# Kernel tuning notes

Measured on AMD Instinct MI355X. Metric: run time of the kernel, lower is better.

Reference implementation:

```python
import jax, jax.numpy as jnp
import numpy as np

ALPHA = 1.0

def setup_inputs() -> dict:
    key = jax.random.key(0)
    kx, kd = jax.random.split(key)
    B, L, D = 64, 256, 512
    x = jax.random.normal(kx, (B, L, D), dtype=jnp.float32)
    duration = jax.random.randint(kd, (B, L), 0, 8, dtype=jnp.int32)
    max_length = 1792  # L * max_duration
    return {"x": x, "duration": duration, "max_length": max_length}

def reference(x, duration, max_length):
    B, L, D = x.shape
    # round(duration * alpha) -> integer durations
    d = jnp.round(duration.astype(jnp.float32) * ALPHA).astype(jnp.int32)
    # rows with all-zero durations get one frame (original picks a random
    # position; we deterministically use position 0)
    row_sum = d.sum(axis=1)  # [B]
    d = jnp.where((row_sum == 0)[:, None] & (jnp.arange(L) == 0)[None, :], 1, d)
    # cumulative end offsets per phoneme: cum[b, j] = sum_{k<=j} d[b, k]
    cum = jnp.cumsum(d, axis=1)  # [B, L]
    t = jnp.arange(max_length)   # [T]
    # output frame t belongs to phoneme j where cum[j-1] <= t < cum[j]
    idx = jax.vmap(lambda c: jnp.searchsorted(c, t, side='right'))(cum)  # [B, T]
    idx = jnp.clip(idx, 0, L - 1)
    out = jnp.take_along_axis(x, idx[:, :, None], axis=1)  # [B, T, D]
    # zero-pad beyond each sequence's total length
    mask = (t[None, :] < cum[:, -1:]).astype(x.dtype)  # [B, T]
    out = out * mask[:, :, None]
    return out, max_length
```

## Files before the change

kernel.cpp:

```cpp
#include <hip/hip_runtime.h>


#define BB 64
#define LL 256
#define DD 512
#define TT 1792
#define D4 (DD / 4)
#define TILE 64
#define NBT (TT / TILE)
#define NBLK (BB * NBT)

typedef float f32x4 __attribute__((ext_vector_type(4)));

__global__ __launch_bounds__(256) void length_regulator_kernel(
    const f32x4* __restrict__ x4,
    const int*   __restrict__ dur,
    const int*   __restrict__ maxlen,
    float*       __restrict__ out)
{
    __shared__ int cum[LL];
    __shared__ int idx_s[TILE];
    const int tid = threadIdx.x;

    const int bid  = blockIdx.x;
    const int virt = (bid & 7) * (NBLK / 8) + (bid >> 3);
    const int b    = virt / NBT;
    const int t0   = (virt % NBT) * TILE;

    cum[tid] = dur[b * LL + tid];
    if (tid < TILE) idx_s[tid] = -1;
    __syncthreads();
    #pragma unroll
    for (int off = 1; off < LL; off <<= 1) {
        int v = (tid >= off) ? cum[tid - off] : 0;
        __syncthreads();
        cum[tid] += v;
        __syncthreads();
    }
    if (cum[LL - 1] == 0) cum[tid] = 1;
    __syncthreads();

    {
        const int end   = cum[tid];
        const int start = (tid > 0) ? cum[tid - 1] : 0;
        const int lo = max(start, t0);
        const int hi = min(end, t0 + TILE);
        for (int t = lo; t < hi; ++t) idx_s[t - t0] = tid;
    }
    __syncthreads();

    const int group = tid >> 7;
    const int lane  = tid & 127;
    const f32x4 z   = (f32x4)(0.f);
    const f32x4* __restrict__ xrow = x4 + (size_t)b * LL * D4;
    f32x4* __restrict__ outb = (f32x4*)out + ((size_t)b * TT + t0) * D4;

    #pragma unroll
    for (int it = 0; it < TILE / 2; ++it) {
        const int toff = it * 2 + group;
        const int id   = idx_s[toff];
        const int idc  = (id >= 0) ? id : 0;
        f32x4 v = xrow[idc * D4 + lane];
        v = (id >= 0) ? v : z;
        __builtin_nontemporal_store(v, outb + toff * D4 + lane);
    }

    if (virt == 0 && tid == 0) {
        out[(size_t)BB * TT * DD] = (float)maxlen[0];
    }
}

extern "C" void kernel_launch(void* const* d_in, const int* in_sizes, int n_in,
                              void* d_out, int out_size, void* d_ws, size_t ws_size,
                              hipStream_t stream) {
    const f32x4* x4  = (const f32x4*)d_in[0];
    const int*   dur = (const int*)d_in[1];
    const int*   ml  = (const int*)d_in[2];
    float*       out = (float*)d_out;

    length_regulator_kernel<<<dim3(NBLK), dim3(256), 0, stream>>>(x4, dur, ml, out);
}
```

Baseline: 269.8 us.

## Use wave-shuffle prefix scan and reuse gathered rows across repeated frames

Replaces the shared-memory Hillis-Steele scan, which needed many barriers, with a wavefront shuffle scan plus a small cross-wave combine. Each 128-thread group now handles a contiguous run of 32 frames and reloads from x only when the phoneme index changes, cutting redundant global loads for repeated frames. Stores switch from nontemporal to ordinary stores. The data-dependent branch in the unrolled loop may serialise the loads, and ordinary stores may pollute the cache with output.

```diff
diff --git a/kernel.cpp b/kernel.cpp
--- a/kernel.cpp
+++ b/kernel.cpp
@@ -18,7 +18,7 @@
     const int*   __restrict__ maxlen,
     float*       __restrict__ out)
 {
-    __shared__ int cum[LL];
+    __shared__ int wsum[4];
     __shared__ int idx_s[TILE];
     const int tid = threadIdx.x;
 
@@ -27,24 +27,27 @@
     const int b    = virt / NBT;
     const int t0   = (virt % NBT) * TILE;
 
-    cum[tid] = dur[b * LL + tid];
+    int d = dur[b * LL + tid];
+    int c = d;
+    #pragma unroll
+    for (int off = 1; off < 64; off <<= 1) {
+        int u = __shfl_up(c, off, 64);
+        if ((tid & 63) >= off) c += u;
+    }
     if (tid < TILE) idx_s[tid] = -1;
+    if ((tid & 63) == 63) wsum[tid >> 6] = c;
     __syncthreads();
-    #pragma unroll
-    for (int off = 1; off < LL; off <<= 1) {
-        int v = (tid >= off) ? cum[tid - off] : 0;
-        __syncthreads();
-        cum[tid] += v;
-        __syncthreads();
+    {
+        const int s0 = wsum[0], s1 = wsum[1], s2 = wsum[2], s3 = wsum[3];
+        const int wid   = tid >> 6;
+        const int total = s0 + s1 + s2 + s3;
+        c += (wid > 0 ? s0 : 0) + (wid > 1 ? s1 : 0) + (wid > 2 ? s2 : 0);
+        if (total == 0) { c = 1; d = (tid == 0) ? 1 : 0; }
     }
-    if (cum[LL - 1] == 0) cum[tid] = 1;
-    __syncthreads();
 
     {
-        const int end   = cum[tid];
-        const int start = (tid > 0) ? cum[tid - 1] : 0;
-        const int lo = max(start, t0);
-        const int hi = min(end, t0 + TILE);
+        const int lo = max(c - d, t0);
+        const int hi = min(c, t0 + TILE);
         for (int t = lo; t < hi; ++t) idx_s[t - t0] = tid;
     }
     __syncthreads();
@@ -55,14 +58,17 @@
     const f32x4* __restrict__ xrow = x4 + (size_t)b * LL * D4;
     f32x4* __restrict__ outb = (f32x4*)out + ((size_t)b * TT + t0) * D4;
 
+    int   prev = -2;
+    f32x4 v    = z;
     #pragma unroll
     for (int it = 0; it < TILE / 2; ++it) {
-        const int toff = it * 2 + group;
+        const int toff = (group << 5) + it;
         const int id   = idx_s[toff];
-        const int idc  = (id >= 0) ? id : 0;
-        f32x4 v = xrow[idc * D4 + lane];
-        v = (id >= 0) ? v : z;
-        __builtin_nontemporal_store(v, outb + toff * D4 + lane);
+        if (id != prev) {
+            v = (id >= 0) ? xrow[id * D4 + lane] : z;
+            prev = id;
+        }
+        outb[toff * D4 + lane] = v;
     }
 
     if (virt == 0 && tid == 0) {
```

Result: no change. 266.0 us (-1.4%).
